# Optimization experiments

Hardware: AMD Instinct MI355X
Metric: run time of the kernel (lower is better)

Reference implementation:

```python
import jax, jax.numpy as jnp
import numpy as np

N_NODES = 100000  # m == n for the square adjacency
LEAKY_SLOPE = 0.5


def setup_inputs() -> dict:
    key = jax.random.key(0)
    k1, k2, k3 = jax.random.split(key, 3)
    E = 3200000
    D = 128
    edge_index = jax.random.randint(k1, (2, E), 0, N_NODES, dtype=jnp.int64)
    edge_vals = jax.random.uniform(k2, (E,), dtype=jnp.float32)
    embeds = jax.random.normal(k3, (N_NODES, D), dtype=jnp.float32)
    return {"edge_index": edge_index, "edge_vals": edge_vals, "embeds": embeds}


def reference(edge_index, edge_vals, embeds):
    # coalesce (sum duplicate (row,col) values) followed by scatter-add SpMM
    # is equivalent to scatter-add SpMM directly on un-coalesced indices.
    row, col = edge_index[0], edge_index[1]
    # gather source embeddings, scale by edge values, segment-sum into rows
    msgs = edge_vals[:, None] * embeds[col]                 # [E, D]
    agg = jax.ops.segment_sum(msgs, row, num_segments=N_NODES)  # [N, D]
    return jax.nn.leaky_relu(agg, negative_slope=LEAKY_SLOPE)
```

## Files before the change

### kernel.cpp

```cpp
#include <hip/hip_runtime.h>
#include <hip/hip_fp16.h>


#define GCN_D       128
#define LEAKY_SLOPE 0.5f
#define NBLK        256
#define RPB         64
#define RPB_SH      6
#define CAP         3072
#define NBINS_MAX   2048
#define SCAN_G      512
#define NCHAIN_FB   4

typedef float    f32x2 __attribute__((ext_vector_type(2)));
typedef float    f32x4 __attribute__((ext_vector_type(4)));
typedef unsigned u32x2 __attribute__((ext_vector_type(2)));
typedef unsigned u32x4 __attribute__((ext_vector_type(4)));

__device__ inline unsigned pack_half2(float a, float b) {
    __half2 h = __floats2half2_rn(a, b);
    return *reinterpret_cast<unsigned*>(&h);
}


__global__ void hist_convert_kernel(const int* __restrict__ row,
                                    int E, int CH, int nbins,
                                    unsigned* __restrict__ hist,
                                    const f32x4* __restrict__ emb4,
                                    int n8,
                                    u32x4* __restrict__ h8) {
    __shared__ unsigned h[NBINS_MAX];
    if ((int)blockIdx.x < NBLK) {
        int b = blockIdx.x;
        for (int i = threadIdx.x; i < nbins; i += blockDim.x) h[i] = 0u;
        __syncthreads();
        int s = b * CH;
        int e = min(E, s + CH);
        for (int i = s + threadIdx.x; i < e; i += blockDim.x)
            atomicAdd(&h[row[i] >> RPB_SH], 1u);
        __syncthreads();
        for (int i = threadIdx.x; i < nbins; i += blockDim.x)
            hist[(long long)i * NBLK + b] = h[i];
    } else {
        int bid = (int)blockIdx.x - NBLK;
        int nb  = (int)gridDim.x - NBLK;
        int stride = nb * blockDim.x;
        for (int i = bid * blockDim.x + threadIdx.x; i < n8; i += stride) {
            f32x4 a  = __builtin_nontemporal_load(&emb4[2 * i]);
            f32x4 b2 = __builtin_nontemporal_load(&emb4[2 * i + 1]);
            u32x4 o;
            o.x = pack_half2(a.x, a.y);
            o.y = pack_half2(a.z, a.w);
            o.z = pack_half2(b2.x, b2.y);
            o.w = pack_half2(b2.z, b2.w);
            h8[i] = o;
        }
    }
}


__global__ void __launch_bounds__(256)
scanA_kernel(const unsigned* __restrict__ data, int M, int chunk,
             unsigned* __restrict__ bsum) {
    __shared__ unsigned red[256];
    int b = blockIdx.x, t = threadIdx.x;
    long long s = (long long)b * chunk;
    unsigned acc = 0;
    for (int i = t; i < chunk; i += 256) {
        long long j = s + i;
        if (j < M) acc += data[j];
    }
    red[t] = acc;
    __syncthreads();
    for (int off = 128; off > 0; off >>= 1) {
        if (t < off) red[t] += red[t + off];
        __syncthreads();
    }
    if (t == 0) bsum[b] = red[0];
}

__global__ void __launch_bounds__(512)
scanB_kernel(unsigned* __restrict__ bsum, int G) {
    __shared__ unsigned s[512];
    int t = threadIdx.x;
    unsigned v = (t < G) ? bsum[t] : 0u;
    s[t] = v;
    __syncthreads();
    for (int off = 1; off < 512; off <<= 1) {
        unsigned u = (t >= off) ? s[t - off] : 0u;
        __syncthreads();
        s[t] += u;
        __syncthreads();
    }
    if (t < G) bsum[t] = (t == 0) ? 0u : s[t - 1];
}

__global__ void __launch_bounds__(256)
scanC_kernel(unsigned* __restrict__ data, int M, int chunk,
             const unsigned* __restrict__ bsum) {
    __shared__ unsigned pre[256];
    int b = blockIdx.x, t = threadIdx.x;
    long long s0 = (long long)b * chunk;
    long long s1 = s0 + chunk;
    int ept = (chunk + 255) / 256;
    long long ts = s0 + (long long)t * ept;

    unsigned acc = 0;
    for (int i = 0; i < ept; ++i) {
        long long j = ts + i;
        if (j < s1 && j < M) acc += data[j];
    }
    pre[t] = acc;
    __syncthreads();
    for (int off = 1; off < 256; off <<= 1) {
        unsigned u = (t >= off) ? pre[t - off] : 0u;
        __syncthreads();
        pre[t] += u;
        __syncthreads();
    }
    unsigned run = bsum[b] + ((t == 0) ? 0u : pre[t - 1]);
    for (int i = 0; i < ept; ++i) {
        long long j = ts + i;
        if (j < s1 && j < M) {
            unsigned v = data[j];
            data[j] = run;
            run += v;
        }
    }
}


__global__ void __launch_bounds__(1024)
scatter_kernel(const int* __restrict__ row,
               const int* __restrict__ col,
               const float* __restrict__ val,
               int E, int CH, int nbins,
               const unsigned* __restrict__ scanned,
               u32x2* __restrict__ entry) {
    __shared__ unsigned cur[NBINS_MAX];
    int b = blockIdx.x;
    for (int i = threadIdx.x; i < nbins; i += blockDim.x)
        cur[i] = scanned[(long long)i * NBLK + b];
    __syncthreads();

    int s = b * CH;
    int e = min(E, s + CH);
    for (int i = s + threadIdx.x; i < e; i += blockDim.x) {
        int r = row[i];
        unsigned key = ((unsigned)(r & (RPB - 1)) << 17) | (unsigned)col[i];
        unsigned pos = atomicAdd(&cur[r >> RPB_SH], 1u);
        u32x2 q; q.x = key; q.y = __float_as_uint(val[i]);
        entry[pos] = q;
    }
}


__global__ void __launch_bounds__(512)
bin_reduce_kernel(const unsigned* __restrict__ scanned,
                  const u32x2* __restrict__ entry,
                  const __half2* __restrict__ ebh,
                  float* __restrict__ out,
                  int E, int N, int nbins) {
    __shared__ u32x2    sorted[CAP];
    __shared__ unsigned cnt[RPB];
    __shared__ unsigned offs[RPB];
    __shared__ unsigned cur[RPB];

    int b    = blockIdx.x;
    int tid  = threadIdx.x;
    int wave = tid >> 6;
    int lane = tid & 63;

    int seg0 = (int)scanned[(long long)b * NBLK];
    int seg1 = (b + 1 < nbins) ? (int)scanned[(long long)(b + 1) * NBLK] : E;

    float ax[8], ay[8];
    #pragma unroll
    for (int j = 0; j < 8; ++j) { ax[j] = 0.f; ay[j] = 0.f; }

    for (int cs = seg0; cs < seg1; cs += CAP) {
        int n = min(CAP, seg1 - cs);

        if (tid < RPB) cnt[tid] = 0u;
        __syncthreads();

        for (int i = tid; i < n; i += 512) {
            u32x2 q = __builtin_nontemporal_load(&entry[cs + i]);
            atomicAdd(&cnt[q.x >> 17], 1u);
        }
        __syncthreads();

        if (wave == 0) {
            unsigned c = cnt[lane];
            unsigned s = c;
            #pragma unroll
            for (int off = 1; off < 64; off <<= 1) {
                unsigned t = __shfl_up(s, off, 64);
                if (lane >= off) s += t;
            }
            offs[lane] = s - c;
            cur[lane]  = s - c;
        }
        __syncthreads();

        for (int i = tid; i < n; i += 512) {
            u32x2 q = __builtin_nontemporal_load(&entry[cs + i]);
            unsigned pos = atomicAdd(&cur[q.x >> 17], 1u);
            sorted[pos] = q;
        }
        __syncthreads();

        #pragma unroll
        for (int j = 0; j < 8; ++j) {
            int r  = (wave << 3) + j;
            int s  = (int)offs[r];
            int en = s + (int)cnt[r];
            int i  = s;
            for (; i + 8 <= en; i += 8) {
                u32x2 q0 = sorted[i],     q1 = sorted[i + 1];
                u32x2 q2 = sorted[i + 2], q3 = sorted[i + 3];
                u32x2 q4 = sorted[i + 4], q5 = sorted[i + 5];
                u32x2 q6 = sorted[i + 6], q7 = sorted[i + 7];
                __half2 m0 = ebh[(long long)(q0.x & 0x1FFFFu) * 64 + lane];
                __half2 m1 = ebh[(long long)(q1.x & 0x1FFFFu) * 64 + lane];
                __half2 m2 = ebh[(long long)(q2.x & 0x1FFFFu) * 64 + lane];
                __half2 m3 = ebh[(long long)(q3.x & 0x1FFFFu) * 64 + lane];
                __half2 m4 = ebh[(long long)(q4.x & 0x1FFFFu) * 64 + lane];
                __half2 m5 = ebh[(long long)(q5.x & 0x1FFFFu) * 64 + lane];
                __half2 m6 = ebh[(long long)(q6.x & 0x1FFFFu) * 64 + lane];
                __half2 m7 = ebh[(long long)(q7.x & 0x1FFFFu) * 64 + lane];
                float2 f;
                f = __half22float2(m0);
                ax[j] += __uint_as_float(q0.y) * f.x; ay[j] += __uint_as_float(q0.y) * f.y;
                f = __half22float2(m1);
                ax[j] += __uint_as_float(q1.y) * f.x; ay[j] += __uint_as_float(q1.y) * f.y;
                f = __half22float2(m2);
                ax[j] += __uint_as_float(q2.y) * f.x; ay[j] += __uint_as_float(q2.y) * f.y;
                f = __half22float2(m3);
                ax[j] += __uint_as_float(q3.y) * f.x; ay[j] += __uint_as_float(q3.y) * f.y;
                f = __half22float2(m4);
                ax[j] += __uint_as_float(q4.y) * f.x; ay[j] += __uint_as_float(q4.y) * f.y;
                f = __half22float2(m5);
                ax[j] += __uint_as_float(q5.y) * f.x; ay[j] += __uint_as_float(q5.y) * f.y;
                f = __half22float2(m6);
                ax[j] += __uint_as_float(q6.y) * f.x; ay[j] += __uint_as_float(q6.y) * f.y;
                f = __half22float2(m7);
                ax[j] += __uint_as_float(q7.y) * f.x; ay[j] += __uint_as_float(q7.y) * f.y;
            }
            for (; i < en; ++i) {
                u32x2 qq = sorted[i];
                __half2 mm = ebh[(long long)(qq.x & 0x1FFFFu) * 64 + lane];
                float2 f = __half22float2(mm);
                ax[j] += __uint_as_float(qq.y) * f.x;
                ay[j] += __uint_as_float(qq.y) * f.y;
            }
        }
        __syncthreads();
    }

    int gr0 = b * RPB + (wave << 3);
    #pragma unroll
    for (int j = 0; j < 8; ++j) {
        int gr = gr0 + j;
        if (gr < N) {
            float x = ax[j], y = ay[j];
            x = x > 0.f ? x : LEAKY_SLOPE * x;
            y = y > 0.f ? y : LEAKY_SLOPE * y;
            f32x2 o; o.x = x; o.y = y;
            __builtin_nontemporal_store(
                o, reinterpret_cast<f32x2*>(out) + (long long)gr * 64 + lane);
        }
    }
}


__global__ void build_nodes_kernel(const int* __restrict__ row,
                                   const int* __restrict__ col,
                                   const float* __restrict__ val,
                                   int E,
                                   int* __restrict__ head,
                                   int4* __restrict__ node) {
    int stride = gridDim.x * blockDim.x;
    for (int i = blockIdx.x * blockDim.x + threadIdx.x; i < E; i += stride) {
        int   r = row[i];
        int   c = col[i];
        float v = val[i];
        int prev = atomicExch(&head[r * NCHAIN_FB + (i & (NCHAIN_FB - 1))], i);
        node[i] = make_int4(prev, c, __float_as_int(v), 0);
    }
}

__global__ void __launch_bounds__(256)
reduce_nodes_kernel(const int* __restrict__ head,
                    const int4* __restrict__ node,
                    const float* __restrict__ embeds,
                    float* __restrict__ out,
                    int N) {
    int wave = (int)((blockIdx.x * (long long)blockDim.x + threadIdx.x) >> 6);
    int lane = threadIdx.x & 63;
    if (wave >= N) return;

    const float2* eb = reinterpret_cast<const float2*>(embeds);
    int4 h = reinterpret_cast<const int4*>(head)[wave];
    int e0 = h.x, e1 = h.y, e2 = h.z, e3 = h.w;

    float ax = 0.f, ay = 0.f;

    while ((e0 & e1 & e2 & e3) != -1) {
        int i0 = e0 >= 0 ? e0 : 0;
        int i1 = e1 >= 0 ? e1 : 0;
        int i2 = e2 >= 0 ? e2 : 0;
        int i3 = e3 >= 0 ? e3 : 0;

        int4 n0 = node[i0];
        int4 n1 = node[i1];
        int4 n2 = node[i2];
        int4 n3 = node[i3];

        int c0 = e0 >= 0 ? n0.y : 0;
        int c1 = e1 >= 0 ? n1.y : 0;
        int c2 = e2 >= 0 ? n2.y : 0;
        int c3 = e3 >= 0 ? n3.y : 0;

        float2 m0 = eb[(long long)c0 * 64 + lane];
        float2 m1 = eb[(long long)c1 * 64 + lane];
        float2 m2 = eb[(long long)c2 * 64 + lane];
        float2 m3 = eb[(long long)c3 * 64 + lane];

        float v0 = e0 >= 0 ? __int_as_float(n0.z) : 0.f;
        float v1 = e1 >= 0 ? __int_as_float(n1.z) : 0.f;
        float v2 = e2 >= 0 ? __int_as_float(n2.z) : 0.f;
        float v3 = e3 >= 0 ? __int_as_float(n3.z) : 0.f;

        ax += v0 * m0.x; ay += v0 * m0.y;
        ax += v1 * m1.x; ay += v1 * m1.y;
        ax += v2 * m2.x; ay += v2 * m2.y;
        ax += v3 * m3.x; ay += v3 * m3.y;

        e0 = e0 >= 0 ? n0.x : -1;
        e1 = e1 >= 0 ? n1.x : -1;
        e2 = e2 >= 0 ? n2.x : -1;
        e3 = e3 >= 0 ? n3.x : -1;
    }

    ax = ax > 0.f ? ax : LEAKY_SLOPE * ax;
    ay = ay > 0.f ? ay : LEAKY_SLOPE * ay;
    reinterpret_cast<float2*>(out)[(long long)wave * 64 + lane] =
        make_float2(ax, ay);
}


__global__ void gcn_scatter_kernel(const int* __restrict__ row_idx,
                                   const int* __restrict__ col_idx,
                                   const float* __restrict__ vals,
                                   const float* __restrict__ embeds,
                                   float* __restrict__ out,
                                   int E) {
    long long tid = (long long)blockIdx.x * blockDim.x + threadIdx.x;
    long long e = tid >> 5;
    if (e >= E) return;
    int q = (int)(tid & 31);
    int row = row_idx[e];
    int col = col_idx[e];
    float v = vals[e];
    const float4* src =
        reinterpret_cast<const float4*>(embeds + (long long)col * GCN_D) + q;
    float4 m = *src;
    float* dst = out + (long long)row * GCN_D + (long long)q * 4;
    atomicAdd(dst + 0, v * m.x);
    atomicAdd(dst + 1, v * m.y);
    atomicAdd(dst + 2, v * m.z);
    atomicAdd(dst + 3, v * m.w);
}

__global__ void gcn_leaky_relu_kernel(float* __restrict__ out, int n4) {
    int i = blockIdx.x * blockDim.x + threadIdx.x;
    if (i >= n4) return;
    float4* p = reinterpret_cast<float4*>(out) + i;
    float4 x = *p;
    x.x = x.x > 0.f ? x.x : LEAKY_SLOPE * x.x;
    x.y = x.y > 0.f ? x.y : LEAKY_SLOPE * x.y;
    x.z = x.z > 0.f ? x.z : LEAKY_SLOPE * x.z;
    x.w = x.w > 0.f ? x.w : LEAKY_SLOPE * x.w;
    *p = x;
}


extern "C" void kernel_launch(void* const* d_in, const int* in_sizes, int n_in,
                              void* d_out, int out_size, void* d_ws, size_t ws_size,
                              hipStream_t stream) {
    const int*   edge_index = (const int*)d_in[0];
    const float* edge_vals  = (const float*)d_in[1];
    const float* embeds     = (const float*)d_in[2];
    float*       out        = (float*)d_out;

    const int E = in_sizes[1];
    const int N = out_size / GCN_D;
    const int* row = edge_index;
    const int* col = edge_index + E;

    const int block = 256;
    const int nbins = (N + RPB - 1) / RPB;
    const int M     = nbins * NBLK;
    const int CH    = (E + NBLK - 1) / NBLK;
    const int chunk = (M + SCAN_G - 1) / SCAN_G;

    size_t hist_b = (((size_t)M * sizeof(unsigned)) + 255) & ~(size_t)255;
    size_t bsum_b = (((size_t)SCAN_G * sizeof(unsigned)) + 255) & ~(size_t)255;
    size_t ent_b  = (((size_t)E * sizeof(u32x2)) + 255) & ~(size_t)255;
    size_t half_b = (size_t)N * GCN_D * sizeof(__half);
    size_t need_r11 = hist_b + bsum_b + ent_b + half_b;

    size_t head_fb = (size_t)N * NCHAIN_FB * sizeof(int);
    size_t need_r3 = head_fb + (size_t)E * sizeof(int4);

    if (ws_size >= need_r11 && nbins <= NBINS_MAX) {
        unsigned* hist  = (unsigned*)d_ws;
        unsigned* bsum  = reinterpret_cast<unsigned*>((char*)d_ws + hist_b);
        u32x2*    entry = reinterpret_cast<u32x2*>((char*)d_ws + hist_b + bsum_b);
        u32x4*    h8    = reinterpret_cast<u32x4*>((char*)d_ws + hist_b + bsum_b + ent_b);

        int n8 = N * (GCN_D / 8);
        int convBlocks = (n8 + block - 1) / block;

        hist_convert_kernel<<<NBLK + convBlocks, block, 0, stream>>>(
            row, E, CH, nbins, hist,
            reinterpret_cast<const f32x4*>(embeds), n8, h8);

        scanA_kernel<<<SCAN_G, 256, 0, stream>>>(hist, M, chunk, bsum);
        scanB_kernel<<<1, 512, 0, stream>>>(bsum, SCAN_G);
        scanC_kernel<<<SCAN_G, 256, 0, stream>>>(hist, M, chunk, bsum);

        scatter_kernel<<<NBLK, 1024, 0, stream>>>(
            row, col, edge_vals, E, CH, nbins, hist, entry);

        bin_reduce_kernel<<<nbins, 512, 0, stream>>>(
            hist, entry, reinterpret_cast<const __half2*>(h8), out, E, N, nbins);
    } else if (ws_size >= need_r3) {
        int*  head = (int*)d_ws;
        int4* node = reinterpret_cast<int4*>((char*)d_ws + head_fb);

        hipMemsetAsync(head, 0xFF, head_fb, stream);
        build_nodes_kernel<<<2048, block, 0, stream>>>(row, col, edge_vals,
                                                       E, head, node);

        long long threads = (long long)N * 64;
        int rblocks = (int)((threads + block - 1) / block);
        reduce_nodes_kernel<<<rblocks, block, 0, stream>>>(
            head, node, embeds, out, N);
    } else {
        hipMemsetAsync(d_out, 0, (size_t)out_size * sizeof(float), stream);
        long long total_threads = (long long)E * 32;
        long long grid = (total_threads + block - 1) / block;
        gcn_scatter_kernel<<<(unsigned)grid, block, 0, stream>>>(
            row, col, edge_vals, embeds, out, E);
        int n4 = out_size / 4;
        gcn_leaky_relu_kernel<<<(n4 + 255) / 256, 256, 0, stream>>>(out, n4);
    }
}
```

Baseline: 195.2 us.

## Fold block-sum scan into scanC, vectorize scatter loads, drop nontemporal loads

Removes the single-block scanB launch by having each scanC block reduce the preceding block sums itself. The scatter kernel now reads row, col and val as 4-wide vectors, which cuts the number of load instructions. Entry reads in bin_reduce switch from nontemporal to normal loads so the second pass over each chunk can hit in cache. The trade-offs are redundant bsum reads in every scanC block and an assumption that row+s is 16-byte aligned, which holds only when CH is a multiple of 4.

```diff
diff --git a/kernel.cpp b/kernel.cpp
--- a/kernel.cpp
+++ b/kernel.cpp
@@ -12,6 +12,7 @@
 #define SCAN_G      512
 #define NCHAIN_FB   4
 
+typedef int      i32x4 __attribute__((ext_vector_type(4)));
 typedef float    f32x2 __attribute__((ext_vector_type(2)));
 typedef float    f32x4 __attribute__((ext_vector_type(4)));
 typedef unsigned u32x2 __attribute__((ext_vector_type(2)));
@@ -79,27 +80,24 @@
     if (t == 0) bsum[b] = red[0];
 }
 
-__global__ void __launch_bounds__(512)
-scanB_kernel(unsigned* __restrict__ bsum, int G) {
-    __shared__ unsigned s[512];
-    int t = threadIdx.x;
-    unsigned v = (t < G) ? bsum[t] : 0u;
-    s[t] = v;
-    __syncthreads();
-    for (int off = 1; off < 512; off <<= 1) {
-        unsigned u = (t >= off) ? s[t - off] : 0u;
-        __syncthreads();
-        s[t] += u;
-        __syncthreads();
-    }
-    if (t < G) bsum[t] = (t == 0) ? 0u : s[t - 1];
-}
-
 __global__ void __launch_bounds__(256)
 scanC_kernel(unsigned* __restrict__ data, int M, int chunk,
              const unsigned* __restrict__ bsum) {
     __shared__ unsigned pre[256];
+    __shared__ unsigned basev;
     int b = blockIdx.x, t = threadIdx.x;
+
+    unsigned acc0 = 0;
+    for (int i = t; i < b; i += 256) acc0 += bsum[i];
+    pre[t] = acc0;
+    __syncthreads();
+    for (int off = 128; off > 0; off >>= 1) {
+        if (t < off) pre[t] += pre[t + off];
+        __syncthreads();
+    }
+    if (t == 0) basev = pre[0];
+    __syncthreads();
+
     long long s0 = (long long)b * chunk;
     long long s1 = s0 + chunk;
     int ept = (chunk + 255) / 256;
@@ -110,6 +108,7 @@
         long long j = ts + i;
         if (j < s1 && j < M) acc += data[j];
     }
+    __syncthreads();
     pre[t] = acc;
     __syncthreads();
     for (int off = 1; off < 256; off <<= 1) {
@@ -118,7 +117,7 @@
         pre[t] += u;
         __syncthreads();
     }
-    unsigned run = bsum[b] + ((t == 0) ? 0u : pre[t - 1]);
+    unsigned run = basev + ((t == 0) ? 0u : pre[t - 1]);
     for (int i = 0; i < ept; ++i) {
         long long j = ts + i;
         if (j < s1 && j < M) {
@@ -145,7 +144,27 @@
 
     int s = b * CH;
     int e = min(E, s + CH);
-    for (int i = s + threadIdx.x; i < e; i += blockDim.x) {
+    int n = e - s;
+    int g4 = n >> 2;
+
+    const i32x4* row4 = reinterpret_cast<const i32x4*>(row + s);
+    const i32x4* col4 = reinterpret_cast<const i32x4*>(col + s);
+    const f32x4* val4 = reinterpret_cast<const f32x4*>(val + s);
+
+    for (int g = threadIdx.x; g < g4; g += 1024) {
+        i32x4 r4 = row4[g];
+        i32x4 c4 = col4[g];
+        f32x4 v4 = val4[g];
+        #pragma unroll
+        for (int k = 0; k < 4; ++k) {
+            int r = r4[k];
+            unsigned key = ((unsigned)(r & (RPB - 1)) << 17) | (unsigned)c4[k];
+            unsigned pos = atomicAdd(&cur[r >> RPB_SH], 1u);
+            u32x2 q; q.x = key; q.y = __float_as_uint(v4[k]);
+            entry[pos] = q;
+        }
+    }
+    for (int i = s + (g4 << 2) + threadIdx.x; i < e; i += 1024) {
         int r = row[i];
         unsigned key = ((unsigned)(r & (RPB - 1)) << 17) | (unsigned)col[i];
         unsigned pos = atomicAdd(&cur[r >> RPB_SH], 1u);
@@ -185,7 +204,7 @@
         __syncthreads();
 
         for (int i = tid; i < n; i += 512) {
-            u32x2 q = __builtin_nontemporal_load(&entry[cs + i]);
+            u32x2 q = entry[cs + i];
             atomicAdd(&cnt[q.x >> 17], 1u);
         }
         __syncthreads();
@@ -204,7 +223,7 @@
         __syncthreads();
 
         for (int i = tid; i < n; i += 512) {
-            u32x2 q = __builtin_nontemporal_load(&entry[cs + i]);
+            u32x2 q = entry[cs + i];
             unsigned pos = atomicAdd(&cur[q.x >> 17], 1u);
             sorted[pos] = q;
         }
@@ -409,12 +428,12 @@
     size_t bsum_b = (((size_t)SCAN_G * sizeof(unsigned)) + 255) & ~(size_t)255;
     size_t ent_b  = (((size_t)E * sizeof(u32x2)) + 255) & ~(size_t)255;
     size_t half_b = (size_t)N * GCN_D * sizeof(__half);
-    size_t need_r11 = hist_b + bsum_b + ent_b + half_b;
+    size_t need_r12 = hist_b + bsum_b + ent_b + half_b;
 
     size_t head_fb = (size_t)N * NCHAIN_FB * sizeof(int);
     size_t need_r3 = head_fb + (size_t)E * sizeof(int4);
 
-    if (ws_size >= need_r11 && nbins <= NBINS_MAX) {
+    if (ws_size >= need_r12 && nbins <= NBINS_MAX) {
         unsigned* hist  = (unsigned*)d_ws;
         unsigned* bsum  = reinterpret_cast<unsigned*>((char*)d_ws + hist_b);
         u32x2*    entry = reinterpret_cast<u32x2*>((char*)d_ws + hist_b + bsum_b);
@@ -428,7 +447,6 @@
             reinterpret_cast<const f32x4*>(embeds), n8, h8);
 
         scanA_kernel<<<SCAN_G, 256, 0, stream>>>(hist, M, chunk, bsum);
-        scanB_kernel<<<1, 512, 0, stream>>>(bsum, SCAN_G);
         scanC_kernel<<<SCAN_G, 256, 0, stream>>>(hist, M, chunk, bsum);
 
         scatter_kernel<<<NBLK, 1024, 0, stream>>>(
```

Result: faster. 188.1 us (-3.7%).
